# Optimization experiments

Measured on AMD Instinct MI355X. Metric: run time of the kernel, lower is better.

## Reference

```python
import jax, jax.numpy as jnp
import numpy as np


def setup_inputs() -> dict:
    key = jax.random.key(0)
    k1, k2, k3, k4 = jax.random.split(key, 4)
    N, IN, OUT, R, B = 8192, 256, 256, 8, 4
    a = jax.random.normal(k1, (N, N), dtype=jnp.float32)
    x = jax.random.normal(k2, (N, IN, R), dtype=jnp.float32)
    w_bases = jax.random.normal(k3, (B, IN, OUT), dtype=jnp.float32) * (1.0 / np.sqrt(IN))
    w_rel = jax.random.normal(k4, (R, B), dtype=jnp.float32) * 0.5
    return {"a": a, "x": x, "w_bases": w_bases, "w_rel": w_rel}


def reference(a, x, w_bases, w_rel):
    # Basis-combined per-relation weights: [R, IN, OUT]
    w = jnp.einsum('rb,bio->rio', w_rel, w_bases)
    # Per-relation aggregation: support_r = a @ x[:, :, r] -> stack as [N, R, IN]
    # (matches torch.cat([a @ x[:,:,r] for r], dim=1) ordering)
    supports = jnp.einsum('nm,mir->nri', a, x)  # [N, R, IN]
    # tmp [N, R*IN] @ weights [R*IN, OUT] fused as one einsum
    out = jnp.einsum('nri,rio->no', supports, w)  # [N, OUT]
    return out
```

## Files before the change

### kernel.cpp

```cpp
#include <hip/hip_runtime.h>
#include <stdint.h>

typedef __fp16 f16x2 __attribute__((ext_vector_type(2)));
typedef __fp16 f16x8 __attribute__((ext_vector_type(8)));
typedef float  f32x4 __attribute__((ext_vector_type(4)));

#define GLOBAL_AS __attribute__((address_space(1)))
#define LDS_AS    __attribute__((address_space(3)))

#define NN   8192
#define INC  256
#define OUTC 256
#define K2   2048
#define YTN  ((size_t)OUTC * NN)

__device__ __forceinline__ void async_copy16(const void* g, void* l) {
    __builtin_amdgcn_global_load_lds((const GLOBAL_AS uint32_t*)g,
                                     (LDS_AS uint32_t*)l, 16, 0, 0);
}

__device__ __forceinline__ f16x8 cvt_f32x8_to_f16x8(f32x4 u0, f32x4 u1) {
    f16x8 out;
    f16x2* p = (f16x2*)&out;
    p[0] = __builtin_amdgcn_cvt_pkrtz(u0[0], u0[1]);
    p[1] = __builtin_amdgcn_cvt_pkrtz(u0[2], u0[3]);
    p[2] = __builtin_amdgcn_cvt_pkrtz(u1[0], u1[1]);
    p[3] = __builtin_amdgcn_cvt_pkrtz(u1[2], u1[3]);
    return out;
}

__global__ void build_w2t16(const float* __restrict__ wb, const float* __restrict__ wr,
                            __fp16* __restrict__ W2T16) {
    int o = blockIdx.x;
    int i = threadIdx.x;
    float s[8];
#pragma unroll
    for (int r = 0; r < 8; ++r) s[r] = 0.f;
#pragma unroll
    for (int b = 0; b < 4; ++b) {
        float w = wb[((size_t)((b << 8) + i)) * OUTC + o];
#pragma unroll
        for (int r = 0; r < 8; ++r) s[r] = fmaf(wr[r * 4 + b], w, s[r]);
    }
    f16x8 out;
    f16x2* p = (f16x2*)&out;
    p[0] = __builtin_amdgcn_cvt_pkrtz(s[0], s[1]);
    p[1] = __builtin_amdgcn_cvt_pkrtz(s[2], s[3]);
    p[2] = __builtin_amdgcn_cvt_pkrtz(s[4], s[5]);
    p[3] = __builtin_amdgcn_cvt_pkrtz(s[6], s[7]);
    *reinterpret_cast<f16x8*>(&W2T16[(size_t)o * K2 + i * 8]) = out;
}

__global__ __launch_bounds__(256, 2)
void gemm1_v3(const __fp16* __restrict__ W2, const float* __restrict__ X,
              float* __restrict__ Cp, int kPerSplit) {
    __shared__ __align__(16) __fp16 As[2][128 * 32];
    __shared__ __align__(16) float  Bs[2][128 * 32];

    const int bm = blockIdx.x * 128;
    const int bn = blockIdx.y * 128;
    const int k0 = blockIdx.z * kPerSplit;

    const int tid  = threadIdx.x;
    const int lane = tid & 63;
    const int wave = tid >> 6;
    const int wm   = (wave >> 1) * 64;
    const int wn   = (wave & 1) * 64;
    const int quad = lane >> 4;
    const int l16  = lane & 15;

    f32x4 acc[4][4];
#pragma unroll
    for (int ti = 0; ti < 4; ++ti)
#pragma unroll
        for (int tj = 0; tj < 4; ++tj)
            acc[ti][tj] = (f32x4){0.f, 0.f, 0.f, 0.f};

    const int nt = kPerSplit / 32;

    auto stageA = [&](int buf, int kc) {
#pragma unroll
        for (int i = 0; i < 2; ++i) {
            int r0 = wave * 32 + i * 16;
            int r  = r0 + (lane >> 2);
            int c  = (lane & 3) ^ ((r >> 1) & 3);
            async_copy16(W2 + (size_t)(bm + r) * K2 + kc + c * 8,
                         (char*)As[buf] + r0 * 64);
        }
    };
    auto stageB = [&](int buf, int kc) {
#pragma unroll
        for (int i = 0; i < 4; ++i) {
            int r0 = wave * 32 + i * 8;
            int r  = r0 + (lane >> 3);
            int c  = (lane & 7) ^ (r & 7);
            async_copy16(X + (size_t)(bn + r) * K2 + kc + (c << 2),
                         (char*)Bs[buf] + r0 * 128);
        }
    };

    stageA(0, k0);
    stageB(0, k0);
    __syncthreads();

    int cur = 0;
    for (int t = 0; t < nt; ++t) {
        if (t + 1 < nt) {
            int kc = k0 + (t + 1) * 32;
            stageA(cur ^ 1, kc);
            stageB(cur ^ 1, kc);
        }
        f16x8 af[4];
#pragma unroll
        for (int j = 0; j < 4; ++j) {
            int row = wm + j * 16 + l16;
            int p   = quad ^ ((row >> 1) & 3);
            af[j] = *(const f16x8*)(&As[cur][0] + row * 32 + p * 8);
        }
        f16x8 bf[4];
#pragma unroll
        for (int j = 0; j < 4; ++j) {
            int row = wn + j * 16 + l16;
            int p0  = (2 * quad)     ^ (row & 7);
            int p1  = (2 * quad + 1) ^ (row & 7);
            f32x4 u0 = *(const f32x4*)(&Bs[cur][0] + row * 32 + p0 * 4);
            f32x4 u1 = *(const f32x4*)(&Bs[cur][0] + row * 32 + p1 * 4);
            bf[j] = cvt_f32x8_to_f16x8(u0, u1);
        }
#pragma unroll
        for (int ti = 0; ti < 4; ++ti)
#pragma unroll
            for (int tj = 0; tj < 4; ++tj)
                acc[ti][tj] = __builtin_amdgcn_mfma_f32_16x16x32_f16(
                    af[ti], bf[tj], acc[ti][tj], 0, 0, 0);
        __syncthreads();
        cur ^= 1;
    }

    float* Cz = Cp + (size_t)blockIdx.z * 256 * NN;
#pragma unroll
    for (int ti = 0; ti < 4; ++ti)
#pragma unroll
        for (int tj = 0; tj < 4; ++tj)
#pragma unroll
            for (int r = 0; r < 4; ++r) {
                int row = bm + wm + ti * 16 + quad * 4 + r;
                int col = bn + wn + tj * 16 + l16;
                Cz[(size_t)row * NN + col] = acc[ti][tj][r];
            }
}

__global__ __launch_bounds__(256, 2)
void gemm2_v3(const float* __restrict__ A, const __fp16* __restrict__ Y,
              float* __restrict__ Cp, int kPerSplit) {
    __shared__ __align__(16) float  As[2][128 * 32];
    __shared__ __align__(16) __fp16 Bs[2][256 * 32];

    const int bm = blockIdx.x * 128;
    const int k0 = blockIdx.z * kPerSplit;

    const int tid  = threadIdx.x;
    const int lane = tid & 63;
    const int wave = tid >> 6;
    const int wm   = (wave >> 1) * 64;
    const int wn   = (wave & 1) * 128;
    const int quad = lane >> 4;
    const int l16  = lane & 15;

    f32x4 acc[4][8];
#pragma unroll
    for (int ti = 0; ti < 4; ++ti)
#pragma unroll
        for (int tj = 0; tj < 8; ++tj)
            acc[ti][tj] = (f32x4){0.f, 0.f, 0.f, 0.f};

    const int nt = kPerSplit / 32;

    auto stageA = [&](int buf, int kc) {
#pragma unroll
        for (int i = 0; i < 4; ++i) {
            int r0 = wave * 32 + i * 8;
            int r  = r0 + (lane >> 3);
            int c  = (lane & 7) ^ (r & 7);
            async_copy16(A + (size_t)(bm + r) * NN + kc + (c << 2),
                         (char*)As[buf] + r0 * 128);
        }
    };
    auto stageB = [&](int buf, int kc) {
#pragma unroll
        for (int i = 0; i < 4; ++i) {
            int r0 = wave * 64 + i * 16;
            int r  = r0 + (lane >> 2);
            int c  = (lane & 3) ^ ((r >> 1) & 3);
            async_copy16(Y + (size_t)r * NN + kc + c * 8,
                         (char*)Bs[buf] + r0 * 64);
        }
    };

    stageA(0, k0);
    stageB(0, k0);
    __syncthreads();

    int cur = 0;
    for (int t = 0; t < nt; ++t) {
        if (t + 1 < nt) {
            int kc = k0 + (t + 1) * 32;
            stageA(cur ^ 1, kc);
            stageB(cur ^ 1, kc);
        }
        f16x8 af[4];
#pragma unroll
        for (int j = 0; j < 4; ++j) {
            int row = wm + j * 16 + l16;
            int p0  = (2 * quad)     ^ (row & 7);
            int p1  = (2 * quad + 1) ^ (row & 7);
            f32x4 u0 = *(const f32x4*)(&As[cur][0] + row * 32 + p0 * 4);
            f32x4 u1 = *(const f32x4*)(&As[cur][0] + row * 32 + p1 * 4);
            af[j] = cvt_f32x8_to_f16x8(u0, u1);
        }
        f16x8 bf[8];
#pragma unroll
        for (int j = 0; j < 8; ++j) {
            int row = wn + j * 16 + l16;
            int p   = quad ^ ((row >> 1) & 3);
            bf[j] = *(const f16x8*)(&Bs[cur][0] + row * 32 + p * 8);
        }
#pragma unroll
        for (int ti = 0; ti < 4; ++ti)
#pragma unroll
            for (int tj = 0; tj < 8; ++tj)
                acc[ti][tj] = __builtin_amdgcn_mfma_f32_16x16x32_f16(
                    af[ti], bf[tj], acc[ti][tj], 0, 0, 0);
        __syncthreads();
        cur ^= 1;
    }

    float* Cz = Cp + (size_t)blockIdx.z * NN * 256;
#pragma unroll
    for (int ti = 0; ti < 4; ++ti)
#pragma unroll
        for (int tj = 0; tj < 8; ++tj)
#pragma unroll
            for (int r = 0; r < 4; ++r) {
                int row = bm + wm + ti * 16 + quad * 4 + r;
                int col = wn + tj * 16 + l16;
                Cz[(size_t)row * 256 + col] = acc[ti][tj][r];
            }
}

__global__ void reduce_yT(const float* __restrict__ yTp, __fp16* __restrict__ yT16) {
    size_t base = ((size_t)blockIdx.x * 256 + threadIdx.x) * 8;
    f32x4 s0 = (f32x4){0.f, 0.f, 0.f, 0.f};
    f32x4 s1 = (f32x4){0.f, 0.f, 0.f, 0.f};
#pragma unroll
    for (int z = 0; z < 4; ++z) {
        const float* p = yTp + (size_t)z * YTN + base;
        s0 += *(const f32x4*)p;
        s1 += *(const f32x4*)(p + 4);
    }
    *reinterpret_cast<f16x8*>(&yT16[base]) = cvt_f32x8_to_f16x8(s0, s1);
}

__global__ void reduce_out(const float* __restrict__ op, float* __restrict__ out) {
    size_t base = ((size_t)blockIdx.x * 256 + threadIdx.x) * 4;
    f32x4 s = (f32x4){0.f, 0.f, 0.f, 0.f};
#pragma unroll
    for (int z = 0; z < 8; ++z)
        s += *(const f32x4*)(op + (size_t)z * YTN + base);
    *reinterpret_cast<f32x4*>(&out[base]) = s;
}

extern "C" void kernel_launch(void* const* d_in, const int* in_sizes, int n_in,
                              void* d_out, int out_size, void* d_ws, size_t ws_size,
                              hipStream_t stream) {
    const float* a  = (const float*)d_in[0];
    const float* x  = (const float*)d_in[1];
    const float* wb = (const float*)d_in[2];
    const float* wr = (const float*)d_in[3];
    float* out = (float*)d_out;

    char* w = (char*)d_ws;
    float*  yT_p  = (float*)(w);
    __fp16* yT16  = (__fp16*)(w + ((size_t)32 << 20));
    float*  out_p = (float*)(w + ((size_t)36 << 20));
    __fp16* W2T16 = (__fp16*)(w + ((size_t)100 << 20));

    build_w2t16<<<dim3(256), dim3(256), 0, stream>>>(wb, wr, W2T16);

    gemm1_v3<<<dim3(2, 64, 4), dim3(256), 0, stream>>>(W2T16, x, yT_p, 512);

    reduce_yT<<<dim3(1024), dim3(256), 0, stream>>>(yT_p, yT16);

    gemm2_v3<<<dim3(64, 1, 8), dim3(256), 0, stream>>>(a, yT16, out_p, 1024);

    reduce_out<<<dim3(2048), dim3(256), 0, stream>>>(out_p, out);
}
```

Measured before the change: 468.5 us.

## Triple-buffer GEMM pipelines with vmcnt waits and halve gemm2 M-tile

```diff
diff --git a/kernel.cpp b/kernel.cpp
--- a/kernel.cpp
+++ b/kernel.cpp
@@ -13,6 +13,9 @@
 #define OUTC 256
 #define K2   2048
 #define YTN  ((size_t)OUTC * NN)
+
+#define WAIT_VMCNT_6() asm volatile("s_waitcnt vmcnt(6)" ::: "memory")
+#define WAIT_VMCNT_0() asm volatile("s_waitcnt vmcnt(0)" ::: "memory")
 
 __device__ __forceinline__ void async_copy16(const void* g, void* l) {
     __builtin_amdgcn_global_load_lds((const GLOBAL_AS uint32_t*)g,
@@ -52,10 +55,10 @@
 }
 
 __global__ __launch_bounds__(256, 2)
-void gemm1_v3(const __fp16* __restrict__ W2, const float* __restrict__ X,
+void gemm1_p3(const __fp16* __restrict__ W2, const float* __restrict__ X,
               float* __restrict__ Cp, int kPerSplit) {
-    __shared__ __align__(16) __fp16 As[2][128 * 32];
-    __shared__ __align__(16) float  Bs[2][128 * 32];
+    __shared__ __align__(16) __fp16 As[3][128 * 32];
+    __shared__ __align__(16) float  Bs[3][128 * 32];
 
     const int bm = blockIdx.x * 128;
     const int bn = blockIdx.y * 128;
@@ -78,7 +81,7 @@
 
     const int nt = kPerSplit / 32;
 
-    auto stageA = [&](int buf, int kc) {
+    auto stage = [&](int buf, int kc) {
 #pragma unroll
         for (int i = 0; i < 2; ++i) {
             int r0 = wave * 32 + i * 16;
@@ -87,8 +90,6 @@
             async_copy16(W2 + (size_t)(bm + r) * K2 + kc + c * 8,
                          (char*)As[buf] + r0 * 64);
         }
-    };
-    auto stageB = [&](int buf, int kc) {
 #pragma unroll
         for (int i = 0; i < 4; ++i) {
             int r0 = wave * 32 + i * 8;
@@ -99,23 +100,13 @@
         }
     };
 
-    stageA(0, k0);
-    stageB(0, k0);
-    __syncthreads();
-
-    int cur = 0;
-    for (int t = 0; t < nt; ++t) {
-        if (t + 1 < nt) {
-            int kc = k0 + (t + 1) * 32;
-            stageA(cur ^ 1, kc);
-            stageB(cur ^ 1, kc);
-        }
+    auto compute = [&](int buf) {
         f16x8 af[4];
 #pragma unroll
         for (int j = 0; j < 4; ++j) {
             int row = wm + j * 16 + l16;
             int p   = quad ^ ((row >> 1) & 3);
-            af[j] = *(const f16x8*)(&As[cur][0] + row * 32 + p * 8);
+            af[j] = *(const f16x8*)(&As[buf][0] + row * 32 + p * 8);
         }
         f16x8 bf[4];
 #pragma unroll
@@ -123,8 +114,8 @@
             int row = wn + j * 16 + l16;
             int p0  = (2 * quad)     ^ (row & 7);
             int p1  = (2 * quad + 1) ^ (row & 7);
-            f32x4 u0 = *(const f32x4*)(&Bs[cur][0] + row * 32 + p0 * 4);
-            f32x4 u1 = *(const f32x4*)(&Bs[cur][0] + row * 32 + p1 * 4);
+            f32x4 u0 = *(const f32x4*)(&Bs[buf][0] + row * 32 + p0 * 4);
+            f32x4 u1 = *(const f32x4*)(&Bs[buf][0] + row * 32 + p1 * 4);
             bf[j] = cvt_f32x8_to_f16x8(u0, u1);
         }
 #pragma unroll
@@ -133,9 +124,21 @@
             for (int tj = 0; tj < 4; ++tj)
                 acc[ti][tj] = __builtin_amdgcn_mfma_f32_16x16x32_f16(
                     af[ti], bf[tj], acc[ti][tj], 0, 0, 0);
-        __syncthreads();
-        cur ^= 1;
+    };
+
+    stage(0, k0);
+    stage(1, k0 + 32);
+
+    int t = 0;
+    for (; t < nt - 1; ++t) {
+        WAIT_VMCNT_6();
+        __builtin_amdgcn_s_barrier();
+        if (t + 2 < nt) stage((t + 2) % 3, k0 + (t + 2) * 32);
+        compute(t % 3);
     }
+    WAIT_VMCNT_0();
+    __builtin_amdgcn_s_barrier();
+    compute((nt - 1) % 3);
 
     float* Cz = Cp + (size_t)blockIdx.z * 256 * NN;
 #pragma unroll
@@ -151,42 +154,40 @@
 }
 
 __global__ __launch_bounds__(256, 2)
-void gemm2_v3(const float* __restrict__ A, const __fp16* __restrict__ Y,
+void gemm2_p3(const float* __restrict__ A, const __fp16* __restrict__ Y,
               float* __restrict__ Cp, int kPerSplit) {
-    __shared__ __align__(16) float  As[2][128 * 32];
-    __shared__ __align__(16) __fp16 Bs[2][256 * 32];
-
-    const int bm = blockIdx.x * 128;
+    __shared__ __align__(16) float  As[3][64 * 32];
+    __shared__ __align__(16) __fp16 Bs[3][256 * 32];
+
+    const int bm = blockIdx.x * 64;
     const int k0 = blockIdx.z * kPerSplit;
 
     const int tid  = threadIdx.x;
     const int lane = tid & 63;
     const int wave = tid >> 6;
-    const int wm   = (wave >> 1) * 64;
+    const int wm   = (wave >> 1) * 32;
     const int wn   = (wave & 1) * 128;
     const int quad = lane >> 4;
     const int l16  = lane & 15;
 
-    f32x4 acc[4][8];
-#pragma unroll
-    for (int ti = 0; ti < 4; ++ti)
+    f32x4 acc[2][8];
+#pragma unroll
+    for (int ti = 0; ti < 2; ++ti)
 #pragma unroll
         for (int tj = 0; tj < 8; ++tj)
             acc[ti][tj] = (f32x4){0.f, 0.f, 0.f, 0.f};
 
     const int nt = kPerSplit / 32;
 
-    auto stageA = [&](int buf, int kc) {
-#pragma unroll
-        for (int i = 0; i < 4; ++i) {
-            int r0 = wave * 32 + i * 8;
+    auto stage = [&](int buf, int kc) {
+#pragma unroll
+        for (int i = 0; i < 2; ++i) {
+            int r0 = wave * 16 + i * 8;
             int r  = r0 + (lane >> 3);
             int c  = (lane & 7) ^ (r & 7);
             async_copy16(A + (size_t)(bm + r) * NN + kc + (c << 2),
                          (char*)As[buf] + r0 * 128);
         }
-    };
-    auto stageB = [&](int buf, int kc) {
 #pragma unroll
         for (int i = 0; i < 4; ++i) {
             int r0 = wave * 64 + i * 16;
@@ -197,25 +198,15 @@
         }
     };
 
-    stageA(0, k0);
-    stageB(0, k0);
-    __syncthreads();
-
-    int cur = 0;
-    for (int t = 0; t < nt; ++t) {
-        if (t + 1 < nt) {
-            int kc = k0 + (t + 1) * 32;
-            stageA(cur ^ 1, kc);
-            stageB(cur ^ 1, kc);
-        }
-        f16x8 af[4];
-#pragma unroll
-        for (int j = 0; j < 4; ++j) {
+    auto compute = [&](int buf) {
+        f16x8 af[2];
+#pragma unroll
+        for (int j = 0; j < 2; ++j) {
             int row = wm + j * 16 + l16;
             int p0  = (2 * quad)     ^ (row & 7);
             int p1  = (2 * quad + 1) ^ (row & 7);
-            f32x4 u0 = *(const f32x4*)(&As[cur][0] + row * 32 + p0 * 4);
-            f32x4 u1 = *(const f32x4*)(&As[cur][0] + row * 32 + p1 * 4);
+            f32x4 u0 = *(const f32x4*)(&As[buf][0] + row * 32 + p0 * 4);
+            f32x4 u1 = *(const f32x4*)(&As[buf][0] + row * 32 + p1 * 4);
             af[j] = cvt_f32x8_to_f16x8(u0, u1);
         }
         f16x8 bf[8];
@@ -223,21 +214,33 @@
         for (int j = 0; j < 8; ++j) {
             int row = wn + j * 16 + l16;
             int p   = quad ^ ((row >> 1) & 3);
-            bf[j] = *(const f16x8*)(&Bs[cur][0] + row * 32 + p * 8);
-        }
-#pragma unroll
-        for (int ti = 0; ti < 4; ++ti)
+            bf[j] = *(const f16x8*)(&Bs[buf][0] + row * 32 + p * 8);
+        }
+#pragma unroll
+        for (int ti = 0; ti < 2; ++ti)
 #pragma unroll
             for (int tj = 0; tj < 8; ++tj)
                 acc[ti][tj] = __builtin_amdgcn_mfma_f32_16x16x32_f16(
                     af[ti], bf[tj], acc[ti][tj], 0, 0, 0);
-        __syncthreads();
-        cur ^= 1;
+    };
+
+    stage(0, k0);
+    stage(1, k0 + 32);
+
+    int t = 0;
+    for (; t < nt - 1; ++t) {
+        WAIT_VMCNT_6();
+        __builtin_amdgcn_s_barrier();
+        if (t + 2 < nt) stage((t + 2) % 3, k0 + (t + 2) * 32);
+        compute(t % 3);
     }
+    WAIT_VMCNT_0();
+    __builtin_amdgcn_s_barrier();
+    compute((nt - 1) % 3);
 
     float* Cz = Cp + (size_t)blockIdx.z * NN * 256;
 #pragma unroll
-    for (int ti = 0; ti < 4; ++ti)
+    for (int ti = 0; ti < 2; ++ti)
 #pragma unroll
         for (int tj = 0; tj < 8; ++tj)
 #pragma unroll
@@ -287,11 +290,11 @@
 
     build_w2t16<<<dim3(256), dim3(256), 0, stream>>>(wb, wr, W2T16);
 
-    gemm1_v3<<<dim3(2, 64, 4), dim3(256), 0, stream>>>(W2T16, x, yT_p, 512);
+    gemm1_p3<<<dim3(2, 64, 4), dim3(256), 0, stream>>>(W2T16, x, yT_p, 512);
 
     reduce_yT<<<dim3(1024), dim3(256), 0, stream>>>(yT_p, yT16);
 
-    gemm2_v3<<<dim3(64, 1, 8), dim3(256), 0, stream>>>(a, yT16, out_p, 1024);
+    gemm2_p3<<<dim3(128, 1, 8), dim3(256), 0, stream>>>(a, yT16, out_p, 1024);
 
     reduce_out<<<dim3(2048), dim3(256), 0, stream>>>(out_p, out);
 }
```

Result: slower. 509.1 us (+8.7%).
